# Kernel optimization log

Measured on AMD Instinct MI355X. Metric: run time of the kernel, lower is better.

## Reference

```python
import jax, jax.numpy as jnp
import numpy as np

U_NUM = 100000
I_NUM = 50000
D = 64
E = 4_000_000
N_LAYERS = 3


def setup_inputs() -> dict:
    key = jax.random.key(0)
    k1, k2, k3, k4 = jax.random.split(key, 4)
    return {
        "user_emb": jax.random.normal(k1, (U_NUM + 1, D), dtype=jnp.float32) * 0.1,
        "item_emb": jax.random.normal(k2, (I_NUM + 1, D), dtype=jnp.float32) * 0.1,
        "edge_user": jax.random.randint(k3, (E,), 0, U_NUM + 1, dtype=jnp.int32),
        "edge_item": jax.random.randint(k4, (E,), 0, I_NUM + 1, dtype=jnp.int32),
    }


def reference(user_emb, item_emb, edge_user, edge_item):
    U = user_emb.shape[0]
    I = item_emb.shape[0]
    N = U + I
    # Symmetrize bipartite interaction edges into full-graph COO indices.
    rows = jnp.concatenate([edge_user, edge_item + U])          # [2E]
    cols = jnp.concatenate([edge_item + U, edge_user])          # [2E]
    # Symmetric degree normalization: A_hat = D^-1/2 A D^-1/2 (deg + 1e-7)
    deg = jax.ops.segment_sum(jnp.ones(rows.shape[0], dtype=jnp.float32), rows, num_segments=N) + 1e-7
    d_inv_sqrt = deg ** -0.5
    vals = d_inv_sqrt[rows] * d_inv_sqrt[cols]                  # [2E]

    emb = jnp.concatenate([user_emb, item_emb], axis=0)         # [N, D]
    acc = emb
    x = emb
    for _ in range(N_LAYERS):
        # SpMM: x_new[r] = sum_{edges (r,c)} vals * x[c]
        x = jax.ops.segment_sum(vals[:, None] * x[cols], rows, num_segments=N)
        acc = acc + x
    total = acc / jnp.float32(N_LAYERS + 1)                     # mean over layer stack
    return total[:U], total[U:]
```

## Files before the change

kernel.cpp:

```cpp
#include <hip/hip_runtime.h>


static constexpr int D = 64;
#define BSHIFT 8
#define BROWS 256
#define KP 1024
#define TILE 2048
#define PADSLACK (7 * BROWS)
#define CSR_LDS_CAP 12288

__device__ __forceinline__ float bflo(unsigned v) {
    unsigned u = v << 16;
    return __builtin_bit_cast(float, u);
}
__device__ __forceinline__ float bfhi(unsigned v) {
    unsigned u = v & 0xFFFF0000u;
    return __builtin_bit_cast(float, u);
}
__device__ __forceinline__ unsigned pack_bf16x2(float a, float b) {
    unsigned ua = __builtin_bit_cast(unsigned, a);
    unsigned ub = __builtin_bit_cast(unsigned, b);
    ua += 0x7FFFu + ((ua >> 16) & 1u);
    ub += 0x7FFFu + ((ub >> 16) & 1u);
    return (ua >> 16) | (ub & 0xFFFF0000u);
}

__device__ __forceinline__ void acc_bf2(unsigned u, float& se, float& so) {
    se += bflo(u);
    so += bfhi(u);
}

__global__ __launch_bounds__(256) void bucket_count(
        const int* __restrict__ eu, const int* __restrict__ ei,
        int* __restrict__ bcnt, int E, int U) {
    __shared__ int h[KP];
    int tid = threadIdx.x;
#pragma unroll
    for (int k = 0; k < 4; ++k) h[tid + k * 256] = 0;
    __syncthreads();
    int E4 = E >> 2;
    int stride = gridDim.x * blockDim.x;
    int g = blockIdx.x * blockDim.x + tid;
    const int4* eu4 = (const int4*)eu;
    const int4* ei4 = (const int4*)ei;
    for (int e = g; e < E4; e += stride) {
        int4 u = eu4[e];
        int4 it = ei4[e];
        atomicAdd(&h[u.x >> BSHIFT], 1);
        atomicAdd(&h[u.y >> BSHIFT], 1);
        atomicAdd(&h[u.z >> BSHIFT], 1);
        atomicAdd(&h[u.w >> BSHIFT], 1);
        atomicAdd(&h[(U + it.x) >> BSHIFT], 1);
        atomicAdd(&h[(U + it.y) >> BSHIFT], 1);
        atomicAdd(&h[(U + it.z) >> BSHIFT], 1);
        atomicAdd(&h[(U + it.w) >> BSHIFT], 1);
    }
    if (blockIdx.x == 0 && tid < (E - (E4 << 2))) {
        int e = (E4 << 2) + tid;
        atomicAdd(&h[eu[e] >> BSHIFT], 1);
        atomicAdd(&h[(U + ei[e]) >> BSHIFT], 1);
    }
    __syncthreads();
#pragma unroll
    for (int k = 0; k < 4; ++k) {
        int v = h[tid + k * 256];
        if (v) atomicAdd(&bcnt[tid + k * 256], v);
    }
}

__global__ void bscan(const int* __restrict__ bcnt, int* __restrict__ bbase,
                      int* __restrict__ bcursor, int KB, int twoE) {
    __shared__ int s[KP];
    int tid = threadIdx.x;
    int v = (tid < KB) ? bcnt[tid] : 0;
    s[tid] = v;
    __syncthreads();
    for (int off = 1; off < KP; off <<= 1) {
        int a = (tid >= off) ? s[tid - off] : 0;
        __syncthreads();
        s[tid] += a;
        __syncthreads();
    }
    int ex = s[tid] - v;
    if (tid < KB) { bbase[tid] = ex; bcursor[tid] = ex; }
    if (tid == KB) bbase[tid] = twoE;
    if (tid > KB) bcursor[tid] = 0;
}

__global__ __launch_bounds__(256) void bucket_scatter(
        const int* __restrict__ eu, const int* __restrict__ ei,
        int* __restrict__ bcursor, unsigned* __restrict__ pairs,
        int E, int U, int twoE) {
    __shared__ int hist[KP];
    __shared__ int sbase[KP];
    __shared__ int gbase[KP];
    __shared__ unsigned staging[TILE];
    __shared__ unsigned short sb[TILE];
    int tid = threadIdx.x;
#pragma unroll
    for (int k = 0; k < 4; ++k) hist[tid + k * 256] = 0;
    __syncthreads();
    int base_e = blockIdx.x * TILE;
    int bk[8]; unsigned pk[8];
#pragma unroll
    for (int k = 0; k < 8; ++k) {
        int e = base_e + k * 256 + tid;
        bk[k] = -1;
        if (e < twoE) {
            int r, c;
            if (e < E) { r = eu[e]; c = U + ei[e]; }
            else       { c = eu[e - E]; r = U + ei[e - E]; }
            int b = r >> BSHIFT;
            bk[k] = b;
            pk[k] = ((unsigned)(r & (BROWS - 1)) << 18) | (unsigned)c;
            atomicAdd(&hist[b], 1);
        }
    }
    __syncthreads();
    int cc[4];
#pragma unroll
    for (int k = 0; k < 4; ++k) cc[k] = hist[tid + k * 256];
    for (int off = 1; off < KP; off <<= 1) {
        int a[4];
#pragma unroll
        for (int k = 0; k < 4; ++k) {
            int idx = tid + k * 256;
            a[k] = (idx >= off) ? hist[idx - off] : 0;
        }
        __syncthreads();
#pragma unroll
        for (int k = 0; k < 4; ++k) hist[tid + k * 256] += a[k];
        __syncthreads();
    }
#pragma unroll
    for (int k = 0; k < 4; ++k) {
        int idx = tid + k * 256;
        int e0 = hist[idx] - cc[k];
        sbase[idx] = e0;
        if (cc[k] > 0) gbase[idx] = atomicAdd(&bcursor[idx], cc[k]);
        hist[idx] = e0;
    }
    __syncthreads();
#pragma unroll
    for (int k = 0; k < 8; ++k) {
        if (bk[k] >= 0) {
            int pos = atomicAdd(&hist[bk[k]], 1);
            staging[pos] = pk[k];
            sb[pos] = (unsigned short)bk[k];
        }
    }
    __syncthreads();
    int tile_n = min(TILE, twoE - base_e);
#pragma unroll
    for (int k = 0; k < 8; ++k) {
        int j = k * 256 + tid;
        if (j < tile_n) {
            int b = sb[j];
            pairs[gbase[b] + (j - sbase[b])] = staging[j];
        }
    }
}

__global__ __launch_bounds__(256) void csr_build(
        const unsigned* __restrict__ pairs, const int* __restrict__ bbase,
        int* __restrict__ deg, int* __restrict__ row_ptr, float* __restrict__ dis,
        int* __restrict__ cols, int N) {
    __shared__ int cnt[BROWS];
    __shared__ int cur[BROWS];
    __shared__ int fin[BROWS];
    __shared__ int lbuf[CSR_LDS_CAP];
    __shared__ int meta[2];
    int tid = threadIdx.x;
    int b = blockIdx.x;
    int lo = bbase[b], hi = bbase[b + 1];
    int cbase = lo + PADSLACK * b;
    cnt[tid] = 0;
    __syncthreads();
    for (int i = lo + tid; i < hi; i += 256) atomicAdd(&cnt[pairs[i] >> 18], 1);
    __syncthreads();
    int c = cnt[tid];
    int p = (c + 7) & ~7;
    cnt[tid] = p;
    __syncthreads();
    for (int off = 1; off < BROWS; off <<= 1) {
        int a = (tid >= off) ? cnt[tid - off] : 0;
        __syncthreads();
        cnt[tid] += a;
        __syncthreads();
    }
    int e = cnt[tid] - p;
    int r = (b << BSHIFT) + tid;
    if (r < N) {
        deg[r] = c;
        row_ptr[r] = cbase + e;
        dis[r] = rsqrtf((float)c + 1e-7f);
    }
    cur[tid] = e;
    fin[tid] = e + p;
    if (tid == 127) meta[0] = cnt[127];
    if (tid == 255) meta[1] = cnt[255];
    __syncthreads();
    int half0 = meta[0];
    int total = meta[1];
    if (half0 <= CSR_LDS_CAP && (total - half0) <= CSR_LDS_CAP) {
#pragma unroll
        for (int half = 0; half < 2; ++half) {
            int base = half ? half0 : 0;
            int end  = half ? total : half0;
            for (int i = lo + tid; i < hi; i += 256) {
                unsigned pe = pairs[i];
                int row = (int)(pe >> 18);
                if ((row >> 7) == half) {
                    int pos = atomicAdd(&cur[row], 1);
                    lbuf[pos - base] = (int)(pe & 0x3FFFFu);
                }
            }
            __syncthreads();
            if ((tid >> 7) == half) {
                for (int i = cur[tid]; i < fin[tid]; ++i) lbuf[i - base] = N;
            }
            __syncthreads();
            for (int i = base + tid; i < end; i += 256)
                cols[cbase + i] = lbuf[i - base];
            __syncthreads();
        }
    } else {
        for (int i = lo + tid; i < hi; i += 256) {
            unsigned pe = pairs[i];
            int pos = atomicAdd(&cur[pe >> 18], 1);
            cols[cbase + pos] = (int)(pe & 0x3FFFFu);
        }
        __syncthreads();
        for (int i = cur[tid]; i < fin[tid]; ++i) cols[cbase + i] = N;
    }
}

__global__ __launch_bounds__(256) void init_kernel(
        const float4* __restrict__ ue4, const float4* __restrict__ ie4,
        const float* __restrict__ dis,
        uint4* __restrict__ xsA4, uint4* __restrict__ xsB4,
        float4* __restrict__ acc4, int U8, int N8) {
    int t = blockIdx.x * blockDim.x + threadIdx.x;
    if (t >= N8 + 8) return;
    if (t >= N8) {
        uint4 z = {0u, 0u, 0u, 0u};
        xsA4[t] = z;
        xsB4[t] = z;
        return;
    }
    float dv = dis[t >> 3];
    const float4* src = (t < U8) ? (ue4 + 2 * t) : (ie4 + 2 * (t - U8));
    float4 a0 = src[0];
    float4 a1 = src[1];
    acc4[2 * t] = a0;
    acc4[2 * t + 1] = a1;
    uint4 w;
    w.x = pack_bf16x2(dv * a0.x, dv * a0.y);
    w.y = pack_bf16x2(dv * a0.z, dv * a0.w);
    w.z = pack_bf16x2(dv * a1.x, dv * a1.y);
    w.w = pack_bf16x2(dv * a1.z, dv * a1.w);
    xsA4[t] = w;
}

__global__ __launch_bounds__(256) void spmm_kernel(
        const int* __restrict__ row_ptr, const int* __restrict__ deg,
        const float* __restrict__ dis, const int* __restrict__ cols,
        const unsigned* __restrict__ xs, unsigned* __restrict__ xs_next,
        float4* __restrict__ acc4, int N, float final_scale) {
    int wid = blockIdx.x * 4 + (threadIdx.x >> 6);
    if (wid >= N) return;
    int lane = threadIdx.x & 63;
    int n8 = lane >> 3;
    int dp = lane & 7;
    int start = row_ptr[wid];
    int cntp = (deg[wid] + 7) & ~7;
    float dr = dis[wid];
    const int* colp = cols + start;
    int vbase = n8 << 2;
    int dpo = dp << 2;
    float s0 = 0.f, s1 = 0.f, s2 = 0.f, s3 = 0.f;
    float s4 = 0.f, s5 = 0.f, s6 = 0.f, s7 = 0.f;
    for (int chunk = 0; chunk < cntp; chunk += 64) {
        int cv = colp[chunk + lane];
        int nq = min(64, cntp - chunk) >> 3;
        nq = __builtin_amdgcn_readfirstlane(nq);
        int coq[8];
        uint4 vq[8];
#pragma unroll
        for (int q = 0; q < 8; ++q) {
            if (q < nq)
                coq[q] = __builtin_amdgcn_ds_bpermute((q << 5) + vbase, cv);
        }
#pragma unroll
        for (int q = 0; q < 8; ++q) {
            if (q < nq)
                vq[q] = *(const uint4*)(xs + (((unsigned)coq[q]) << 5) + dpo);
        }
#pragma unroll
        for (int q = 0; q < 8; ++q) {
            if (q < nq) {
                acc_bf2(vq[q].x, s0, s1);
                acc_bf2(vq[q].y, s2, s3);
                acc_bf2(vq[q].z, s4, s5);
                acc_bf2(vq[q].w, s6, s7);
            }
        }
    }
#pragma unroll
    for (int m = 8; m < 64; m <<= 1) {
        s0 += __shfl_xor(s0, m); s1 += __shfl_xor(s1, m);
        s2 += __shfl_xor(s2, m); s3 += __shfl_xor(s3, m);
        s4 += __shfl_xor(s4, m); s5 += __shfl_xor(s5, m);
        s6 += __shfl_xor(s6, m); s7 += __shfl_xor(s7, m);
    }
    if (n8 == 0) {
        float x0 = dr * s0, x1 = dr * s1, x2 = dr * s2, x3 = dr * s3;
        float x4 = dr * s4, x5 = dr * s5, x6 = dr * s6, x7 = dr * s7;
        uint4 w;
        w.x = pack_bf16x2(dr * x0, dr * x1);
        w.y = pack_bf16x2(dr * x2, dr * x3);
        w.z = pack_bf16x2(dr * x4, dr * x5);
        w.w = pack_bf16x2(dr * x6, dr * x7);
        ((uint4*)xs_next)[(wid << 3) + dp] = w;
        int o = (wid << 4) + (dp << 1);
        float4 a = acc4[o];
        a.x = (a.x + x0) * final_scale;
        a.y = (a.y + x1) * final_scale;
        a.z = (a.z + x2) * final_scale;
        a.w = (a.w + x3) * final_scale;
        acc4[o] = a;
        float4 b2 = acc4[o + 1];
        b2.x = (b2.x + x4) * final_scale;
        b2.y = (b2.y + x5) * final_scale;
        b2.z = (b2.z + x6) * final_scale;
        b2.w = (b2.w + x7) * final_scale;
        acc4[o + 1] = b2;
    }
}

extern "C" void kernel_launch(void* const* d_in, const int* in_sizes, int n_in,
                              void* d_out, int out_size, void* d_ws, size_t ws_size,
                              hipStream_t stream) {
    const float* ue = (const float*)d_in[0];
    const float* ie = (const float*)d_in[1];
    const int* eu = (const int*)d_in[2];
    const int* ei = (const int*)d_in[3];
    const int U = in_sizes[0] / D;
    const int I = in_sizes[1] / D;
    const int N = U + I;
    const int E = in_sizes[2];
    const int twoE = 2 * E;
    const int KB = (N + BROWS - 1) / BROWS;
    float* out = (float*)d_out;

    char* ws = (char*)d_ws;
    auto alloc = [&](size_t bytes) {
        char* p = ws;
        ws += (bytes + 255) & ~(size_t)255;
        return p;
    };
    int* deg = (int*)alloc((size_t)N * 4);
    int* row_ptr = (int*)alloc((size_t)N * 4);
    float* dis = (float*)alloc((size_t)N * 4);
    int* bcnt = (int*)alloc(KP * 4);
    int* bbase = (int*)alloc((KP + 1) * 4);
    int* bcursor = (int*)alloc(KP * 4);
    int* cols = (int*)alloc(((size_t)twoE + (size_t)PADSLACK * (KB + 1) + 256) * 4);
    unsigned* pairs = (unsigned*)alloc((size_t)twoE * 4);
    unsigned* xsA = (unsigned*)alloc(((size_t)N + 1) * 32 * 4);
    unsigned* xsB = (unsigned*)alloc(((size_t)N + 1) * 32 * 4);

    hipMemsetAsync(bcnt, 0, KP * 4, stream);
    bucket_count<<<1024, 256, 0, stream>>>(eu, ei, bcnt, E, U);
    bscan<<<1, KP, 0, stream>>>(bcnt, bbase, bcursor, KB, twoE);
    bucket_scatter<<<(twoE + TILE - 1) / TILE, 256, 0, stream>>>(
        eu, ei, bcursor, pairs, E, U, twoE);
    csr_build<<<KB, BROWS, 0, stream>>>(pairs, bbase, deg, row_ptr, dis, cols, N);

    int N8 = N * 8, U8 = U * 8;
    init_kernel<<<(N8 + 8 + 255) / 256, 256, 0, stream>>>(
        (const float4*)ue, (const float4*)ie, dis,
        (uint4*)xsA, (uint4*)xsB, (float4*)out, U8, N8);

    unsigned* x = xsA;
    unsigned* xn = xsB;
    for (int l = 0; l < 3; ++l) {
        float fs = (l == 2) ? 0.25f : 1.0f;
        spmm_kernel<<<(N + 3) / 4, 256, 0, stream>>>(
            row_ptr, deg, dis, cols, x, xn, (float4*)out, N, fs);
        unsigned* tmp = x; x = xn; xn = tmp;
    }
}
```

Baseline: 639.1 us.

## Map eight rows per wavefront in SpMM, one row per 8-lane group

The SpMM kernel now gives each 8-lane group its own row instead of spreading one row across a whole wavefront. Each group loads column indices four at a time and gathers bf16 feature vectors directly, which removes the ds_bpermute broadcast and the cross-lane shuffle reduction at the end. Rows with fewer neighbours are padded with the dummy row N, and the loop runs to the largest padded degree within the wavefront. The intent is to cut shuffle overhead and give better occupancy for low-degree rows. The trade-off is divergence when degrees within a wavefront differ, plus extra slack in the column buffer for the vector loads.

Result: slower. 694.4 us (+8.7%).

```diff
diff --git a/kernel.cpp b/kernel.cpp
--- a/kernel.cpp
+++ b/kernel.cpp
@@ -8,6 +8,7 @@
 #define TILE 2048
 #define PADSLACK (7 * BROWS)
 #define CSR_LDS_CAP 12288
+#define COLS_SLACK 8192
 
 __device__ __forceinline__ float bflo(unsigned v) {
     unsigned u = v << 16;
@@ -268,52 +269,45 @@
         const unsigned* __restrict__ xs, unsigned* __restrict__ xs_next,
         float4* __restrict__ acc4, int N, float final_scale) {
     int wid = blockIdx.x * 4 + (threadIdx.x >> 6);
-    if (wid >= N) return;
     int lane = threadIdx.x & 63;
-    int n8 = lane >> 3;
+    int o = lane >> 3;
     int dp = lane & 7;
-    int start = row_ptr[wid];
-    int cntp = (deg[wid] + 7) & ~7;
-    float dr = dis[wid];
+    int r = wid * 8 + o;
+    int rc = min(r, N - 1);
+    int start = row_ptr[rc];
+    int dg = deg[rc];
+    float dr = dis[rc];
+    int cntp = (r < N) ? ((dg + 7) & ~7) : 0;
+    int mx = cntp;
+    mx = max(mx, __shfl_xor(mx, 8));
+    mx = max(mx, __shfl_xor(mx, 16));
+    mx = max(mx, __shfl_xor(mx, 32));
     const int* colp = cols + start;
-    int vbase = n8 << 2;
-    int dpo = dp << 2;
+    unsigned dpo = (unsigned)(dp << 2);
     float s0 = 0.f, s1 = 0.f, s2 = 0.f, s3 = 0.f;
     float s4 = 0.f, s5 = 0.f, s6 = 0.f, s7 = 0.f;
-    for (int chunk = 0; chunk < cntp; chunk += 64) {
-        int cv = colp[chunk + lane];
-        int nq = min(64, cntp - chunk) >> 3;
-        nq = __builtin_amdgcn_readfirstlane(nq);
-        int coq[8];
-        uint4 vq[8];
-#pragma unroll
-        for (int q = 0; q < 8; ++q) {
-            if (q < nq)
-                coq[q] = __builtin_amdgcn_ds_bpermute((q << 5) + vbase, cv);
-        }
-#pragma unroll
-        for (int q = 0; q < 8; ++q) {
-            if (q < nq)
-                vq[q] = *(const uint4*)(xs + (((unsigned)coq[q]) << 5) + dpo);
-        }
-#pragma unroll
-        for (int q = 0; q < 8; ++q) {
-            if (q < nq) {
-                acc_bf2(vq[q].x, s0, s1);
-                acc_bf2(vq[q].y, s2, s3);
-                acc_bf2(vq[q].z, s4, s5);
-                acc_bf2(vq[q].w, s6, s7);
-            }
-        }
-    }
-#pragma unroll
-    for (int m = 8; m < 64; m <<= 1) {
-        s0 += __shfl_xor(s0, m); s1 += __shfl_xor(s1, m);
-        s2 += __shfl_xor(s2, m); s3 += __shfl_xor(s3, m);
-        s4 += __shfl_xor(s4, m); s5 += __shfl_xor(s5, m);
-        s6 += __shfl_xor(s6, m); s7 += __shfl_xor(s7, m);
-    }
-    if (n8 == 0) {
+    for (int k4 = 0; k4 < mx; k4 += 4) {
+        bool act = (k4 < cntp);
+        int kk = act ? k4 : 0;
+        uint4 cq = *(const uint4*)(colp + kk);
+        unsigned c0 = act ? cq.x : (unsigned)N;
+        unsigned c1 = act ? cq.y : (unsigned)N;
+        unsigned c2 = act ? cq.z : (unsigned)N;
+        unsigned c3 = act ? cq.w : (unsigned)N;
+        uint4 v0 = *(const uint4*)(xs + (c0 << 5) + dpo);
+        uint4 v1 = *(const uint4*)(xs + (c1 << 5) + dpo);
+        uint4 v2 = *(const uint4*)(xs + (c2 << 5) + dpo);
+        uint4 v3 = *(const uint4*)(xs + (c3 << 5) + dpo);
+        acc_bf2(v0.x, s0, s1); acc_bf2(v0.y, s2, s3);
+        acc_bf2(v0.z, s4, s5); acc_bf2(v0.w, s6, s7);
+        acc_bf2(v1.x, s0, s1); acc_bf2(v1.y, s2, s3);
+        acc_bf2(v1.z, s4, s5); acc_bf2(v1.w, s6, s7);
+        acc_bf2(v2.x, s0, s1); acc_bf2(v2.y, s2, s3);
+        acc_bf2(v2.z, s4, s5); acc_bf2(v2.w, s6, s7);
+        acc_bf2(v3.x, s0, s1); acc_bf2(v3.y, s2, s3);
+        acc_bf2(v3.z, s4, s5); acc_bf2(v3.w, s6, s7);
+    }
+    if (r < N) {
         float x0 = dr * s0, x1 = dr * s1, x2 = dr * s2, x3 = dr * s3;
         float x4 = dr * s4, x5 = dr * s5, x6 = dr * s6, x7 = dr * s7;
         uint4 w;
@@ -321,20 +315,20 @@
         w.y = pack_bf16x2(dr * x2, dr * x3);
         w.z = pack_bf16x2(dr * x4, dr * x5);
         w.w = pack_bf16x2(dr * x6, dr * x7);
-        ((uint4*)xs_next)[(wid << 3) + dp] = w;
-        int o = (wid << 4) + (dp << 1);
-        float4 a = acc4[o];
+        ((uint4*)xs_next)[(r << 3) + dp] = w;
+        int oo = (r << 4) + (dp << 1);
+        float4 a = acc4[oo];
         a.x = (a.x + x0) * final_scale;
         a.y = (a.y + x1) * final_scale;
         a.z = (a.z + x2) * final_scale;
         a.w = (a.w + x3) * final_scale;
-        acc4[o] = a;
-        float4 b2 = acc4[o + 1];
+        acc4[oo] = a;
+        float4 b2 = acc4[oo + 1];
         b2.x = (b2.x + x4) * final_scale;
         b2.y = (b2.y + x5) * final_scale;
         b2.z = (b2.z + x6) * final_scale;
         b2.w = (b2.w + x7) * final_scale;
-        acc4[o + 1] = b2;
+        acc4[oo + 1] = b2;
     }
 }
 
@@ -365,7 +359,7 @@
     int* bcnt = (int*)alloc(KP * 4);
     int* bbase = (int*)alloc((KP + 1) * 4);
     int* bcursor = (int*)alloc(KP * 4);
-    int* cols = (int*)alloc(((size_t)twoE + (size_t)PADSLACK * (KB + 1) + 256) * 4);
+    int* cols = (int*)alloc(((size_t)twoE + (size_t)PADSLACK * (KB + 1) + COLS_SLACK) * 4);
     unsigned* pairs = (unsigned*)alloc((size_t)twoE * 4);
     unsigned* xsA = (unsigned*)alloc(((size_t)N + 1) * 32 * 4);
     unsigned* xsB = (unsigned*)alloc(((size_t)N + 1) * 32 * 4);
@@ -384,9 +378,11 @@
 
     unsigned* x = xsA;
     unsigned* xn = xsB;
+    int nwaves = (N + 7) / 8;
+    int nblocks = (nwaves + 3) / 4;
     for (int l = 0; l < 3; ++l) {
         float fs = (l == 2) ? 0.25f : 1.0f;
-        spmm_kernel<<<(N + 3) / 4, 256, 0, stream>>>(
+        spmm_kernel<<<nblocks, 256, 0, stream>>>(
             row_ptr, deg, dis, cols, x, xn, (float4*)out, N, fs);
         unsigned* tmp = x; x = xn; xn = tmp;
     }
```

## Replace fp32 accumulator read-modify-write with fp16 layer snapshots summed in final layer

Applied to the files above, without the earlier changes.

The running fp32 accumulator that each SpMM layer read and rewrote is removed. The two middle layers now store their per-layer outputs as fp16 snapshots, one of them placed in the reused pairs buffer. The last layer reads the original embeddings and both snapshots to write the mean directly. This is meant to cut output traffic: the 256 B/row fp32 read-modify-write per layer becomes a 128 B fp16 write per middle layer and reads only in the final layer, at the cost of fp16 precision for the intermediate layer terms.

Result: faster. 620.1 us (-3.0%).

```diff
diff --git a/kernel.cpp b/kernel.cpp
--- a/kernel.cpp
+++ b/kernel.cpp
@@ -8,6 +8,7 @@
 #define TILE 2048
 #define PADSLACK (7 * BROWS)
 #define CSR_LDS_CAP 12288
+#define COLS_SLACK 8192
 
 __device__ __forceinline__ float bflo(unsigned v) {
     unsigned u = v << 16;
@@ -23,6 +24,17 @@
     ua += 0x7FFFu + ((ua >> 16) & 1u);
     ub += 0x7FFFu + ((ub >> 16) & 1u);
     return (ua >> 16) | (ub & 0xFFFF0000u);
+}
+__device__ __forceinline__ unsigned pack_f16x2(float a, float b) {
+    unsigned short ua = __builtin_bit_cast(unsigned short, (_Float16)a);
+    unsigned short ub = __builtin_bit_cast(unsigned short, (_Float16)b);
+    return (unsigned)ua | ((unsigned)ub << 16);
+}
+__device__ __forceinline__ float f16lo(unsigned v) {
+    return (float)__builtin_bit_cast(_Float16, (unsigned short)(v & 0xFFFFu));
+}
+__device__ __forceinline__ float f16hi(unsigned v) {
+    return (float)__builtin_bit_cast(_Float16, (unsigned short)(v >> 16));
 }
 
 __device__ __forceinline__ void acc_bf2(unsigned u, float& se, float& so) {
@@ -239,7 +251,7 @@
         const float4* __restrict__ ue4, const float4* __restrict__ ie4,
         const float* __restrict__ dis,
         uint4* __restrict__ xsA4, uint4* __restrict__ xsB4,
-        float4* __restrict__ acc4, int U8, int N8) {
+        int U8, int N8) {
     int t = blockIdx.x * blockDim.x + threadIdx.x;
     if (t >= N8 + 8) return;
     if (t >= N8) {
@@ -252,8 +264,6 @@
     const float4* src = (t < U8) ? (ue4 + 2 * t) : (ie4 + 2 * (t - U8));
     float4 a0 = src[0];
     float4 a1 = src[1];
-    acc4[2 * t] = a0;
-    acc4[2 * t + 1] = a1;
     uint4 w;
     w.x = pack_bf16x2(dv * a0.x, dv * a0.y);
     w.y = pack_bf16x2(dv * a0.z, dv * a0.w);
@@ -262,11 +272,11 @@
     xsA4[t] = w;
 }
 
-__global__ __launch_bounds__(256) void spmm_kernel(
+__global__ __launch_bounds__(256) void spmm_mid(
         const int* __restrict__ row_ptr, const int* __restrict__ deg,
         const float* __restrict__ dis, const int* __restrict__ cols,
         const unsigned* __restrict__ xs, unsigned* __restrict__ xs_next,
-        float4* __restrict__ acc4, int N, float final_scale) {
+        unsigned* __restrict__ xh, int N) {
     int wid = blockIdx.x * 4 + (threadIdx.x >> 6);
     if (wid >= N) return;
     int lane = threadIdx.x & 63;
@@ -322,19 +332,89 @@
         w.z = pack_bf16x2(dr * x4, dr * x5);
         w.w = pack_bf16x2(dr * x6, dr * x7);
         ((uint4*)xs_next)[(wid << 3) + dp] = w;
-        int o = (wid << 4) + (dp << 1);
-        float4 a = acc4[o];
-        a.x = (a.x + x0) * final_scale;
-        a.y = (a.y + x1) * final_scale;
-        a.z = (a.z + x2) * final_scale;
-        a.w = (a.w + x3) * final_scale;
-        acc4[o] = a;
-        float4 b2 = acc4[o + 1];
-        b2.x = (b2.x + x4) * final_scale;
-        b2.y = (b2.y + x5) * final_scale;
-        b2.z = (b2.z + x6) * final_scale;
-        b2.w = (b2.w + x7) * final_scale;
-        acc4[o + 1] = b2;
+        uint4 h;
+        h.x = pack_f16x2(x0, x1);
+        h.y = pack_f16x2(x2, x3);
+        h.z = pack_f16x2(x4, x5);
+        h.w = pack_f16x2(x6, x7);
+        ((uint4*)xh)[(wid << 3) + dp] = h;
+    }
+}
+
+__global__ __launch_bounds__(256) void spmm_last(
+        const int* __restrict__ row_ptr, const int* __restrict__ deg,
+        const float* __restrict__ dis, const int* __restrict__ cols,
+        const unsigned* __restrict__ xs,
+        const float4* __restrict__ ue4, const float4* __restrict__ ie4,
+        const unsigned* __restrict__ xh1, const unsigned* __restrict__ xh2,
+        float4* __restrict__ out4, int U, int N) {
+    int wid = blockIdx.x * 4 + (threadIdx.x >> 6);
+    if (wid >= N) return;
+    int lane = threadIdx.x & 63;
+    int n8 = lane >> 3;
+    int dp = lane & 7;
+    int start = row_ptr[wid];
+    int cntp = (deg[wid] + 7) & ~7;
+    float dr = dis[wid];
+    const int* colp = cols + start;
+    int vbase = n8 << 2;
+    int dpo = dp << 2;
+    float s0 = 0.f, s1 = 0.f, s2 = 0.f, s3 = 0.f;
+    float s4 = 0.f, s5 = 0.f, s6 = 0.f, s7 = 0.f;
+    for (int chunk = 0; chunk < cntp; chunk += 64) {
+        int cv = colp[chunk + lane];
+        int nq = min(64, cntp - chunk) >> 3;
+        nq = __builtin_amdgcn_readfirstlane(nq);
+        int coq[8];
+        uint4 vq[8];
+#pragma unroll
+        for (int q = 0; q < 8; ++q) {
+            if (q < nq)
+                coq[q] = __builtin_amdgcn_ds_bpermute((q << 5) + vbase, cv);
+        }
+#pragma unroll
+        for (int q = 0; q < 8; ++q) {
+            if (q < nq)
+                vq[q] = *(const uint4*)(xs + (((unsigned)coq[q]) << 5) + dpo);
+        }
+#pragma unroll
+        for (int q = 0; q < 8; ++q) {
+            if (q < nq) {
+                acc_bf2(vq[q].x, s0, s1);
+                acc_bf2(vq[q].y, s2, s3);
+                acc_bf2(vq[q].z, s4, s5);
+                acc_bf2(vq[q].w, s6, s7);
+            }
+        }
+    }
+#pragma unroll
+    for (int m = 8; m < 64; m <<= 1) {
+        s0 += __shfl_xor(s0, m); s1 += __shfl_xor(s1, m);
+        s2 += __shfl_xor(s2, m); s3 += __shfl_xor(s3, m);
+        s4 += __shfl_xor(s4, m); s5 += __shfl_xor(s5, m);
+        s6 += __shfl_xor(s6, m); s7 += __shfl_xor(s7, m);
+    }
+    if (n8 == 0) {
+        float x30 = dr * s0, x31 = dr * s1, x32 = dr * s2, x33 = dr * s3;
+        float x34 = dr * s4, x35 = dr * s5, x36 = dr * s6, x37 = dr * s7;
+        const float4* ep = (wid < U) ? (ue4 + (size_t)wid * 16)
+                                     : (ie4 + (size_t)(wid - U) * 16);
+        float4 e0 = ep[2 * dp];
+        float4 e1 = ep[2 * dp + 1];
+        uint4 h1 = ((const uint4*)xh1)[(wid << 3) + dp];
+        uint4 h2 = ((const uint4*)xh2)[(wid << 3) + dp];
+        float4 o0, o1;
+        o0.x = 0.25f * (e0.x + f16lo(h1.x) + f16lo(h2.x) + x30);
+        o0.y = 0.25f * (e0.y + f16hi(h1.x) + f16hi(h2.x) + x31);
+        o0.z = 0.25f * (e0.z + f16lo(h1.y) + f16lo(h2.y) + x32);
+        o0.w = 0.25f * (e0.w + f16hi(h1.y) + f16hi(h2.y) + x33);
+        o1.x = 0.25f * (e1.x + f16lo(h1.z) + f16lo(h2.z) + x34);
+        o1.y = 0.25f * (e1.y + f16hi(h1.z) + f16hi(h2.z) + x35);
+        o1.z = 0.25f * (e1.z + f16lo(h1.w) + f16lo(h2.w) + x36);
+        o1.w = 0.25f * (e1.w + f16hi(h1.w) + f16hi(h2.w) + x37);
+        int oo = (wid << 4) + (dp << 1);
+        out4[oo] = o0;
+        out4[oo + 1] = o1;
     }
 }
 
@@ -365,10 +445,12 @@
     int* bcnt = (int*)alloc(KP * 4);
     int* bbase = (int*)alloc((KP + 1) * 4);
     int* bcursor = (int*)alloc(KP * 4);
-    int* cols = (int*)alloc(((size_t)twoE + (size_t)PADSLACK * (KB + 1) + 256) * 4);
+    int* cols = (int*)alloc(((size_t)twoE + (size_t)PADSLACK * (KB + 1) + COLS_SLACK) * 4);
     unsigned* pairs = (unsigned*)alloc((size_t)twoE * 4);
     unsigned* xsA = (unsigned*)alloc(((size_t)N + 1) * 32 * 4);
     unsigned* xsB = (unsigned*)alloc(((size_t)N + 1) * 32 * 4);
+    unsigned* xh1 = pairs;
+    unsigned* xh2 = (unsigned*)alloc((size_t)N * 32 * 4);
 
     hipMemsetAsync(bcnt, 0, KP * 4, stream);
     bucket_count<<<1024, 256, 0, stream>>>(eu, ei, bcnt, E, U);
@@ -380,14 +462,14 @@
     int N8 = N * 8, U8 = U * 8;
     init_kernel<<<(N8 + 8 + 255) / 256, 256, 0, stream>>>(
         (const float4*)ue, (const float4*)ie, dis,
-        (uint4*)xsA, (uint4*)xsB, (float4*)out, U8, N8);
-
-    unsigned* x = xsA;
-    unsigned* xn = xsB;
-    for (int l = 0; l < 3; ++l) {
-        float fs = (l == 2) ? 0.25f : 1.0f;
-        spmm_kernel<<<(N + 3) / 4, 256, 0, stream>>>(
-            row_ptr, deg, dis, cols, x, xn, (float4*)out, N, fs);
-        unsigned* tmp = x; x = xn; xn = tmp;
-    }
-}
+        (uint4*)xsA, (uint4*)xsB, U8, N8);
+
+    int nblocks = (N + 3) / 4;
+    spmm_mid<<<nblocks, 256, 0, stream>>>(
+        row_ptr, deg, dis, cols, xsA, xsB, xh1, N);
+    spmm_mid<<<nblocks, 256, 0, stream>>>(
+        row_ptr, deg, dis, cols, xsB, xsA, xh2, N);
+    spmm_last<<<nblocks, 256, 0, stream>>>(
+        row_ptr, deg, dis, cols, xsA,
+        (const float4*)ue, (const float4*)ie, xh1, xh2, (float4*)out, U, N);
+}
```
